# Performance work log

Measured on AMD Instinct MI355X. Metric: run time of the kernel, lower is better.

The kernel has to match this reference:

```python
import jax, jax.numpy as jnp
import numpy as np

TAU_MEM = 20.0
V_THRESH = 1.0
DECAY = float(np.exp(-1.0 / TAU_MEM))
SLOPE = 5.0  # fast-sigmoid surrogate slope


@jax.custom_vjp
def spike(x):
    # Heaviside spike with fast-sigmoid surrogate gradient
    return (x > 0).astype(x.dtype)

def _spike_fwd(x):
    return spike(x), x

def _spike_bwd(x, g):
    surr = 1.0 / (1.0 + SLOPE * jnp.abs(x)) ** 2
    return (g * surr,)

spike.defvjp(_spike_fwd, _spike_bwd)


def setup_inputs() -> dict:
    key = jax.random.key(0)
    k1, k2 = jax.random.split(key)
    B, T, n_in, n_out = 32, 1000, 1024, 512
    input_spikes_seq = (jax.random.uniform(k1, (B, T, n_in)) < 0.05).astype(jnp.float32)
    w_init_scale = 0.5
    W = jax.random.normal(k2, (n_out, n_in), dtype=jnp.float32) * (w_init_scale / np.sqrt(n_in))
    return {"input_spikes_seq": input_spikes_seq, "W": W}


def reference(input_spikes_seq, W):
    # input_spikes_seq: (B, T, n_in); W: (n_out, n_in) -> out: (B, T, n_out)
    B, T, _ = input_spikes_seq.shape
    n_out = W.shape[0]
    # Hoist the GEMM out of the time loop: (B,T,n_in) x (n_out,n_in) -> (B,T,n_out)
    I = jnp.einsum('bti,oi->bto', input_spikes_seq, W)
    I_t = jnp.transpose(I, (1, 0, 2))  # (T, B, n_out)

    def step(v, i_t):
        v = v * DECAY + i_t
        s = spike(v - V_THRESH)
        v = v * (1.0 - jax.lax.stop_gradient(s))  # reset, detached as in torch
        return v, s

    v0 = jnp.zeros((B, n_out), dtype=input_spikes_seq.dtype)
    _, out_t = jax.lax.scan(step, v0, I_t)  # out_t: (T, B, n_out)
    return jnp.transpose(out_t, (1, 0, 2))
```

## Files before the change

kernel.cpp:

```cpp
#include <hip/hip_runtime.h>


#define N_IN   1024
#define N_OUT  512
#define DECAY_F 0.95122942450071400910f
#define SCALE     17179869184.0
#define SCALE_INV 5.8207660913467407e-11f

typedef int  v4i  __attribute__((ext_vector_type(4)));
typedef int  v16i __attribute__((ext_vector_type(16)));

typedef __attribute__((address_space(1))) const void gv_t;
typedef __attribute__((address_space(3))) void lv_t;
__device__ __forceinline__ void gl16(const signed char* g, signed char* l) {
    __builtin_amdgcn_global_load_lds((gv_t*)g, (lv_t*)l, 16, 0, 0);
}

__global__ __launch_bounds__(256) void prep(const float* __restrict__ S,
                                            signed char* __restrict__ S8,
                                            const float* __restrict__ W,
                                            signed char* __restrict__ D8,
                                            int nS16blocks) {
    if ((int)blockIdx.x < nS16blocks) {
        const int g = blockIdx.x * 256 + threadIdx.x;
        const float4* p = reinterpret_cast<const float4*>(S) + (size_t)g * 4;
        union { signed char c[16]; int4 v; } u;
#pragma unroll
        for (int q = 0; q < 4; ++q) {
            const float4 v = p[q];
            u.c[q * 4 + 0] = (signed char)(v.x != 0.f);
            u.c[q * 4 + 1] = (signed char)(v.y != 0.f);
            u.c[q * 4 + 2] = (signed char)(v.z != 0.f);
            u.c[q * 4 + 3] = (signed char)(v.w != 0.f);
        }
        reinterpret_cast<int4*>(S8)[g] = u.v;
    } else {
        const int n  = blockIdx.x - nS16blocks;
        const int k0 = threadIdx.x * 4;
        const float4 wv = *reinterpret_cast<const float4*>(W + (size_t)n * N_IN + k0);
        const float ww[4] = {wv.x, wv.y, wv.z, wv.w};
        int pk[4] = {0, 0, 0, 0};
#pragma unroll
        for (int j = 0; j < 4; ++j) {
            long long wi = (long long)rint((double)ww[j] * SCALE);
            const int d0 = (int)((wi + 128) & 255) - 128; wi = (wi - d0) >> 8;
            const int d1 = (int)((wi + 128) & 255) - 128; wi = (wi - d1) >> 8;
            const int d2 = (int)((wi + 128) & 255) - 128; wi = (wi - d2) >> 8;
            const int d3 = (int)wi;
            pk[0] |= (d0 & 255) << (8 * j);
            pk[1] |= (d1 & 255) << (8 * j);
            pk[2] |= (d2 & 255) << (8 * j);
            pk[3] |= (d3 & 255) << (8 * j);
        }
#pragma unroll
        for (int d = 0; d < 4; ++d)
            *reinterpret_cast<int*>(D8 + (size_t)(d * N_OUT + n) * N_IN + k0) = pk[d];
    }
}

#define BM 256
#define BN 64
#define BK 64
#define TILEB (BM * BK)
#define BUFSZ (2 * TILEB)

#define BARRIER __builtin_amdgcn_s_barrier()
#define LGKM0 do { asm volatile("s_waitcnt lgkmcnt(0)" ::: "memory");             \
                   __builtin_amdgcn_sched_barrier(0); } while (0)
#define VMCNT_(n) asm volatile("s_waitcnt vmcnt(" #n ")" ::: "memory")
#define LDV(off) (*reinterpret_cast<const v4i*>(lds + (off)))
#define MFMA_I8 __builtin_amdgcn_mfma_i32_32x32x32_i8

__global__ __launch_bounds__(512, 2) void gemm_i8(
        const signed char* __restrict__ S8,
        const signed char* __restrict__ D8,
        float* __restrict__ I, int M) {
    extern __shared__ signed char lds[];

    const int tid  = threadIdx.x;
    const int lane = tid & 63;
    const int w    = tid >> 6;
    const int wwm  = w >> 1;
    const int wwn  = w & 1;

    const int nx  = M / BM;
    const int u   = (blockIdx.x & 7) * nx + (blockIdx.x >> 3);
    const int bm  = u >> 3;
    const int bn  = u & 7;
    const int m0 = bm * BM;
    const int n0 = bn * BN;

    const int lrow  = lane >> 2;
    const int sslot = (lane & 3) << 4;
    const int swzs  = ((lrow >> 1) & 3) << 4;
    const int scola = sslot ^ swzs;

    const signed char* aSrc0 = S8 + (size_t)(m0 + w * 16 + lrow) * N_IN + scola;
    const signed char* aSrc1 = aSrc0 + (size_t)128 * N_IN;
    const signed char* bSrc0 = D8 + (size_t)((w >> 2) * N_OUT + n0 + (w & 3) * 16 + lrow) * N_IN + scola;
    const signed char* bSrc1 = bSrc0 + (size_t)2 * N_OUT * N_IN;

    const int aDst0 = (w * 16) * 64;
    const int aDst1 = aDst0 + 128 * 64;
    const int bDst0 = TILEB + (w * 16) * 64;
    const int bDst1 = bDst0 + 128 * 64;

    v16i acc[2][4];
#pragma unroll
    for (int mf = 0; mf < 2; ++mf)
#pragma unroll
        for (int d = 0; d < 4; ++d)
#pragma unroll
            for (int i = 0; i < 16; ++i) acc[mf][d][i] = 0;

    const int fr = lane & 31;
    const int kh = (lane >> 5) * 16;
    const int swzr = ((fr >> 1) & 3) << 4;
    const int kx0 = kh ^ swzr;
    const int kx1 = (32 + kh) ^ swzr;
    const int ra0 = (wwm * 64 + fr) * 64;
    const int ra1 = (wwm * 64 + 32 + fr) * 64;
    const int rb0 = (0 * 64 + wwn * 32 + fr) * 64;
    const int rb1 = (1 * 64 + wwn * 32 + fr) * 64;
    const int rb2 = (2 * 64 + wwn * 32 + fr) * 64;
    const int rb3 = (3 * 64 + wwn * 32 + fr) * 64;

#define TILE_STEP(CUR, STG, KT, DOSTAGE, VML)                                     \
    {                                                                             \
        const int base = (CUR) * BUFSZ;                                           \
        v4i af0, af1, bf0, bf1, bf2, bf3;                                         \
                                                           \
        af0 = LDV(base + ra0 + kx0);                                              \
        af1 = LDV(base + ra1 + kx0);                                              \
        bf0 = LDV(base + TILEB + rb0 + kx0);                                      \
        bf1 = LDV(base + TILEB + rb1 + kx0);                                      \
        bf2 = LDV(base + TILEB + rb2 + kx0);                                      \
        bf3 = LDV(base + TILEB + rb3 + kx0);                                      \
        if (DOSTAGE) {                                                            \
            gl16(aSrc0 + (KT + 2) * BK, lds + (STG) * BUFSZ + aDst0);             \
            gl16(aSrc1 + (KT + 2) * BK, lds + (STG) * BUFSZ + aDst1);             \
        }                                                                         \
        LGKM0;                                                                    \
        __builtin_amdgcn_s_setprio(1);                                            \
        acc[0][0] = MFMA_I8(af0, bf0, acc[0][0], 0, 0, 0);                        \
        acc[1][0] = MFMA_I8(af1, bf0, acc[1][0], 0, 0, 0);                        \
        acc[0][1] = MFMA_I8(af0, bf1, acc[0][1], 0, 0, 0);                        \
        acc[1][1] = MFMA_I8(af1, bf1, acc[1][1], 0, 0, 0);                        \
        acc[0][2] = MFMA_I8(af0, bf2, acc[0][2], 0, 0, 0);                        \
        acc[1][2] = MFMA_I8(af1, bf2, acc[1][2], 0, 0, 0);                        \
        acc[0][3] = MFMA_I8(af0, bf3, acc[0][3], 0, 0, 0);                        \
        acc[1][3] = MFMA_I8(af1, bf3, acc[1][3], 0, 0, 0);                        \
        __builtin_amdgcn_s_setprio(0);                                            \
                                                           \
        af0 = LDV(base + ra0 + kx1);                                              \
        af1 = LDV(base + ra1 + kx1);                                              \
        bf0 = LDV(base + TILEB + rb0 + kx1);                                      \
        bf1 = LDV(base + TILEB + rb1 + kx1);                                      \
        bf2 = LDV(base + TILEB + rb2 + kx1);                                      \
        bf3 = LDV(base + TILEB + rb3 + kx1);                                      \
        if (DOSTAGE) {                                                            \
            gl16(bSrc0 + (KT + 2) * BK, lds + (STG) * BUFSZ + bDst0);             \
            gl16(bSrc1 + (KT + 2) * BK, lds + (STG) * BUFSZ + bDst1);             \
        }                                                                         \
        LGKM0;                                                                    \
        __builtin_amdgcn_s_setprio(1);                                            \
        acc[0][0] = MFMA_I8(af0, bf0, acc[0][0], 0, 0, 0);                        \
        acc[1][0] = MFMA_I8(af1, bf0, acc[1][0], 0, 0, 0);                        \
        acc[0][1] = MFMA_I8(af0, bf1, acc[0][1], 0, 0, 0);                        \
        acc[1][1] = MFMA_I8(af1, bf1, acc[1][1], 0, 0, 0);                        \
        acc[0][2] = MFMA_I8(af0, bf2, acc[0][2], 0, 0, 0);                        \
        acc[1][2] = MFMA_I8(af1, bf2, acc[1][2], 0, 0, 0);                        \
        acc[0][3] = MFMA_I8(af0, bf3, acc[0][3], 0, 0, 0);                        \
        acc[1][3] = MFMA_I8(af1, bf3, acc[1][3], 0, 0, 0);                        \
        __builtin_amdgcn_s_setprio(0);                                            \
        VMCNT_(VML);                                                              \
        BARRIER;                                                                  \
    }

    gl16(aSrc0, lds + aDst0);
    gl16(aSrc1, lds + aDst1);
    gl16(bSrc0, lds + bDst0);
    gl16(bSrc1, lds + bDst1);
    gl16(aSrc0 + BK, lds + BUFSZ + aDst0);
    gl16(aSrc1 + BK, lds + BUFSZ + aDst1);
    gl16(bSrc0 + BK, lds + BUFSZ + bDst0);
    gl16(bSrc1 + BK, lds + BUFSZ + bDst1);
    VMCNT_(4);
    BARRIER;

    TILE_STEP(0, 2, 0,  1, 4)
    TILE_STEP(1, 0, 1,  1, 4)
    TILE_STEP(2, 1, 2,  1, 4)
    TILE_STEP(0, 2, 3,  1, 4)
    TILE_STEP(1, 0, 4,  1, 4)
    TILE_STEP(2, 1, 5,  1, 4)
    TILE_STEP(0, 2, 6,  1, 4)
    TILE_STEP(1, 0, 7,  1, 4)
    TILE_STEP(2, 1, 8,  1, 4)
    TILE_STEP(0, 2, 9,  1, 4)
    TILE_STEP(1, 0, 10, 1, 4)
    TILE_STEP(2, 1, 11, 1, 4)
    TILE_STEP(0, 2, 12, 1, 4)
    TILE_STEP(1, 0, 13, 1, 4)
    TILE_STEP(2, 1, 14, 0, 0)
    TILE_STEP(0, 0, 15, 0, 0)

    const int col = fr;
    const int rb_ = (lane >> 5) * 4;
#pragma unroll
    for (int mf = 0; mf < 2; ++mf) {
#pragma unroll
        for (int reg = 0; reg < 16; ++reg) {
            const int row = (reg & 3) + 8 * (reg >> 2) + rb_;
            const long long v =
                ((long long)acc[mf][3][reg] << 24) + ((long long)acc[mf][2][reg] << 16) +
                ((long long)acc[mf][1][reg] << 8) + (long long)acc[mf][0][reg];
            I[(size_t)(m0 + wwm * 64 + mf * 32 + row) * N_OUT + n0 + wwn * 32 + col] =
                (float)v * SCALE_INV;
        }
    }
}
#undef TILE_STEP

#define UT 50
__global__ __launch_bounds__(64) void lif_scan3(float* __restrict__ IO, int T) {
    const int idx = blockIdx.x * 64 + threadIdx.x;
    const int b = idx >> 9, o = idx & (N_OUT - 1);
    float* p = IO + (size_t)b * T * N_OUT + o;
    float ca[UT], cb[UT];
    float v = 0.f;
#pragma unroll
    for (int j = 0; j < UT; ++j) ca[j] = p[(size_t)j * N_OUT];
#pragma unroll 1
    for (int t0 = 0; t0 < T; t0 += 2 * UT) {
        if (t0 + UT < T) {
#pragma unroll
            for (int j = 0; j < UT; ++j) cb[j] = p[(size_t)(t0 + UT + j) * N_OUT];
        }
#pragma unroll
        for (int j = 0; j < UT; ++j) {
            v = v * DECAY_F + ca[j];
            float s = (v > 1.0f) ? 1.0f : 0.f;
            v *= (1.f - s);
            ca[j] = s;
        }
#pragma unroll
        for (int j = 0; j < UT; ++j) p[(size_t)(t0 + j) * N_OUT] = ca[j];
        if (t0 + UT >= T) break;
        if (t0 + 2 * UT < T) {
#pragma unroll
            for (int j = 0; j < UT; ++j) ca[j] = p[(size_t)(t0 + 2 * UT + j) * N_OUT];
        }
#pragma unroll
        for (int j = 0; j < UT; ++j) {
            v = v * DECAY_F + cb[j];
            float s = (v > 1.0f) ? 1.0f : 0.f;
            v *= (1.f - s);
            cb[j] = s;
        }
#pragma unroll
        for (int j = 0; j < UT; ++j) p[(size_t)(t0 + UT + j) * N_OUT] = cb[j];
    }
}

__global__ __launch_bounds__(256) void transpose_w(const float* __restrict__ W,
                                                   float* __restrict__ WT) {
    __shared__ float t[32][33];
    const int k0 = blockIdx.x * 32;
    const int n0 = blockIdx.y * 32;
    const int lx = threadIdx.x & 31;
    const int ly = threadIdx.x >> 5;
#pragma unroll
    for (int r = ly; r < 32; r += 8)
        t[r][lx] = W[(size_t)(n0 + r) * N_IN + k0 + lx];
    __syncthreads();
#pragma unroll
    for (int r = ly; r < 32; r += 8)
        WT[(size_t)(k0 + r) * N_OUT + n0 + lx] = t[lx][r];
}

__global__ __launch_bounds__(256) void gather_rows(
        const float* __restrict__ S, const float* __restrict__ WT,
        float* __restrict__ I, int M) {
    const int wid  = blockIdx.x * 4 + (threadIdx.x >> 6);
    const int lane = threadIdx.x & 63;
    if (wid >= M) return;
    const float* srow = S + (size_t)wid * N_IN;
    float4 a0 = {0.f, 0.f, 0.f, 0.f};
    float4 a1 = {0.f, 0.f, 0.f, 0.f};
    float sv[16];
#pragma unroll
    for (int g = 0; g < 16; ++g) sv[g] = srow[g * 64 + lane];
#pragma unroll
    for (int g = 0; g < 16; ++g) {
        unsigned long long m = __ballot(sv[g] != 0.0f);
        while (m) {
            const int bb = __builtin_ctzll(m);
            m &= m - 1;
            const int k = g * 64 + bb;
            const float* wp = WT + (size_t)k * N_OUT + lane * 4;
            const float4 w0 = *reinterpret_cast<const float4*>(wp);
            const float4 w1 = *reinterpret_cast<const float4*>(wp + 256);
            a0.x += w0.x; a0.y += w0.y; a0.z += w0.z; a0.w += w0.w;
            a1.x += w1.x; a1.y += w1.y; a1.z += w1.z; a1.w += w1.w;
        }
    }
    float* op = I + (size_t)wid * N_OUT + lane * 4;
    *reinterpret_cast<float4*>(op) = a0;
    *reinterpret_cast<float4*>(op + 256) = a1;
}

extern "C" void kernel_launch(void* const* d_in, const int* in_sizes, int n_in,
                              void* d_out, int out_size, void* d_ws, size_t ws_size,
                              hipStream_t stream) {
    const float* S = (const float*)d_in[0];
    const float* W = (const float*)d_in[1];
    float* out = (float*)d_out;

    const int K = N_IN;
    const int M = in_sizes[0] / K;
    const int B = 32;
    const int T = M / B;

    const size_t s8_bytes = (size_t)M * N_IN;
    const size_t d8_bytes = (size_t)4 * N_OUT * N_IN;
    const size_t need = s8_bytes + d8_bytes;

    if (ws_size >= need && (M % BM) == 0 && ((M / BM) * (N_OUT / BN)) % 8 == 0) {
        signed char* S8 = (signed char*)d_ws;
        signed char* D8 = (signed char*)d_ws + s8_bytes;
        const int nS16blocks = (M * N_IN / 16) / 256;
        prep<<<nS16blocks + N_OUT, 256, 0, stream>>>(S, S8, W, D8, nS16blocks);
        const size_t lds_bytes = (size_t)3 * BUFSZ;
        gemm_i8<<<(M / BM) * (N_OUT / BN), 512, lds_bytes, stream>>>(S8, D8, out, M);
        lif_scan3<<<(B * N_OUT) / 64, 64, 0, stream>>>(out, T);
    } else if (ws_size >= (size_t)N_IN * N_OUT * sizeof(float) && (M % 4) == 0) {
        float* WT = (float*)d_ws;
        dim3 tg(N_IN / 32, N_OUT / 32);
        transpose_w<<<tg, 256, 0, stream>>>(W, WT);
        gather_rows<<<M / 4, 256, 0, stream>>>(S, WT, out, M);
        lif_scan3<<<(B * N_OUT) / 64, 64, 0, stream>>>(out, T);
    }
}
```

Baseline: 140.5 us.

## Split weights into three int8 digits instead of four to cut MFMA work

Lowers the fixed-point weight scale from 2^34 to 2^26, so each weight splits into three signed int8 digits instead of four. The B tile shrinks to 192 rows, the MFMA count per K-step drops by a quarter, and one global load per wave in the upper half of the block is skipped. The LDS fragment loads are also reordered: both K-halves are issued up front and a partial lgkmcnt wait lets the first MFMA batch start earlier. Weight quantisation becomes coarser (resolution about 1.5e-8), which could flip spikes whose membrane potential sits right at threshold.

```diff
diff --git a/kernel.cpp b/kernel.cpp
--- a/kernel.cpp
+++ b/kernel.cpp
@@ -4,8 +4,8 @@
 #define N_IN   1024
 #define N_OUT  512
 #define DECAY_F 0.95122942450071400910f
-#define SCALE     17179869184.0
-#define SCALE_INV 5.8207660913467407e-11f
+#define SCALE     67108864.0
+#define SCALE_INV 1.4901161193847656e-08f
 
 typedef int  v4i  __attribute__((ext_vector_type(4)));
 typedef int  v16i __attribute__((ext_vector_type(16)));
@@ -39,21 +39,19 @@
         const int k0 = threadIdx.x * 4;
         const float4 wv = *reinterpret_cast<const float4*>(W + (size_t)n * N_IN + k0);
         const float ww[4] = {wv.x, wv.y, wv.z, wv.w};
-        int pk[4] = {0, 0, 0, 0};
+        int pk[3] = {0, 0, 0};
 #pragma unroll
         for (int j = 0; j < 4; ++j) {
             long long wi = (long long)rint((double)ww[j] * SCALE);
             const int d0 = (int)((wi + 128) & 255) - 128; wi = (wi - d0) >> 8;
             const int d1 = (int)((wi + 128) & 255) - 128; wi = (wi - d1) >> 8;
-            const int d2 = (int)((wi + 128) & 255) - 128; wi = (wi - d2) >> 8;
-            const int d3 = (int)wi;
+            const int d2 = (int)wi;
             pk[0] |= (d0 & 255) << (8 * j);
             pk[1] |= (d1 & 255) << (8 * j);
             pk[2] |= (d2 & 255) << (8 * j);
-            pk[3] |= (d3 & 255) << (8 * j);
-        }
-#pragma unroll
-        for (int d = 0; d < 4; ++d)
+        }
+#pragma unroll
+        for (int d = 0; d < 3; ++d)
             *reinterpret_cast<int*>(D8 + (size_t)(d * N_OUT + n) * N_IN + k0) = pk[d];
     }
 }
@@ -61,13 +59,15 @@
 #define BM 256
 #define BN 64
 #define BK 64
-#define TILEB (BM * BK)
-#define BUFSZ (2 * TILEB)
+#define ATILE (BM * BK)
+#define BTILE (192 * BK)
+#define BUFSZ (ATILE + BTILE)
 
 #define BARRIER __builtin_amdgcn_s_barrier()
-#define LGKM0 do { asm volatile("s_waitcnt lgkmcnt(0)" ::: "memory");             \
-                   __builtin_amdgcn_sched_barrier(0); } while (0)
+#define SB0 __builtin_amdgcn_sched_barrier(0)
+#define LGKM(n) do { asm volatile("s_waitcnt lgkmcnt(" #n ")" ::: "memory"); SB0; } while (0)
 #define VMCNT_(n) asm volatile("s_waitcnt vmcnt(" #n ")" ::: "memory")
+#define VMC do { if (w < 4) VMCNT_(4); else VMCNT_(3); } while (0)
 #define LDV(off) (*reinterpret_cast<const v4i*>(lds + (off)))
 #define MFMA_I8 __builtin_amdgcn_mfma_i32_32x32x32_i8
 
@@ -102,14 +102,14 @@
 
     const int aDst0 = (w * 16) * 64;
     const int aDst1 = aDst0 + 128 * 64;
-    const int bDst0 = TILEB + (w * 16) * 64;
+    const int bDst0 = ATILE + (w * 16) * 64;
     const int bDst1 = bDst0 + 128 * 64;
 
-    v16i acc[2][4];
+    v16i acc[2][3];
 #pragma unroll
     for (int mf = 0; mf < 2; ++mf)
 #pragma unroll
-        for (int d = 0; d < 4; ++d)
+        for (int d = 0; d < 3; ++d)
 #pragma unroll
             for (int i = 0; i < 16; ++i) acc[mf][d][i] = 0;
 
@@ -123,87 +123,81 @@
     const int rb0 = (0 * 64 + wwn * 32 + fr) * 64;
     const int rb1 = (1 * 64 + wwn * 32 + fr) * 64;
     const int rb2 = (2 * 64 + wwn * 32 + fr) * 64;
-    const int rb3 = (3 * 64 + wwn * 32 + fr) * 64;
-
-#define TILE_STEP(CUR, STG, KT, DOSTAGE, VML)                                     \
+
+#define TILE_STEP(CUR, STG, KT, DOSTAGE)                                          \
     {                                                                             \
         const int base = (CUR) * BUFSZ;                                           \
-        v4i af0, af1, bf0, bf1, bf2, bf3;                                         \
-                                                           \
-        af0 = LDV(base + ra0 + kx0);                                              \
-        af1 = LDV(base + ra1 + kx0);                                              \
-        bf0 = LDV(base + TILEB + rb0 + kx0);                                      \
-        bf1 = LDV(base + TILEB + rb1 + kx0);                                      \
-        bf2 = LDV(base + TILEB + rb2 + kx0);                                      \
-        bf3 = LDV(base + TILEB + rb3 + kx0);                                      \
+        v4i xa0, xa1, xb0, xb1, xb2;                                              \
+        v4i ya0, ya1, yb0, yb1, yb2;                                              \
+        xa0 = LDV(base + ra0 + kx0);                                              \
+        xa1 = LDV(base + ra1 + kx0);                                              \
+        xb0 = LDV(base + ATILE + rb0 + kx0);                                      \
+        xb1 = LDV(base + ATILE + rb1 + kx0);                                      \
+        xb2 = LDV(base + ATILE + rb2 + kx0);                                      \
+        SB0;                                                                      \
+        ya0 = LDV(base + ra0 + kx1);                                              \
+        ya1 = LDV(base + ra1 + kx1);                                              \
+        yb0 = LDV(base + ATILE + rb0 + kx1);                                      \
+        yb1 = LDV(base + ATILE + rb1 + kx1);                                      \
+        yb2 = LDV(base + ATILE + rb2 + kx1);                                      \
+        SB0;                                                                      \
+        LGKM(5);                                                                  \
         if (DOSTAGE) {                                                            \
             gl16(aSrc0 + (KT + 2) * BK, lds + (STG) * BUFSZ + aDst0);             \
             gl16(aSrc1 + (KT + 2) * BK, lds + (STG) * BUFSZ + aDst1);             \
         }                                                                         \
-        LGKM0;                                                                    \
         __builtin_amdgcn_s_setprio(1);                                            \
-        acc[0][0] = MFMA_I8(af0, bf0, acc[0][0], 0, 0, 0);                        \
-        acc[1][0] = MFMA_I8(af1, bf0, acc[1][0], 0, 0, 0);                        \
-        acc[0][1] = MFMA_I8(af0, bf1, acc[0][1], 0, 0, 0);                        \
-        acc[1][1] = MFMA_I8(af1, bf1, acc[1][1], 0, 0, 0);                        \
-        acc[0][2] = MFMA_I8(af0, bf2, acc[0][2], 0, 0, 0);                        \
-        acc[1][2] = MFMA_I8(af1, bf2, acc[1][2], 0, 0, 0);                        \
-        acc[0][3] = MFMA_I8(af0, bf3, acc[0][3], 0, 0, 0);                        \
-        acc[1][3] = MFMA_I8(af1, bf3, acc[1][3], 0, 0, 0);                        \
+        acc[0][0] = MFMA_I8(xa0, xb0, acc[0][0], 0, 0, 0);                        \
+        acc[1][0] = MFMA_I8(xa1, xb0, acc[1][0], 0, 0, 0);                        \
+        acc[0][1] = MFMA_I8(xa0, xb1, acc[0][1], 0, 0, 0);                        \
+        acc[1][1] = MFMA_I8(xa1, xb1, acc[1][1], 0, 0, 0);                        \
+        acc[0][2] = MFMA_I8(xa0, xb2, acc[0][2], 0, 0, 0);                        \
+        acc[1][2] = MFMA_I8(xa1, xb2, acc[1][2], 0, 0, 0);                        \
         __builtin_amdgcn_s_setprio(0);                                            \
-                                                           \
-        af0 = LDV(base + ra0 + kx1);                                              \
-        af1 = LDV(base + ra1 + kx1);                                              \
-        bf0 = LDV(base + TILEB + rb0 + kx1);                                      \
-        bf1 = LDV(base + TILEB + rb1 + kx1);                                      \
-        bf2 = LDV(base + TILEB + rb2 + kx1);                                      \
-        bf3 = LDV(base + TILEB + rb3 + kx1);                                      \
         if (DOSTAGE) {                                                            \
             gl16(bSrc0 + (KT + 2) * BK, lds + (STG) * BUFSZ + bDst0);             \
-            gl16(bSrc1 + (KT + 2) * BK, lds + (STG) * BUFSZ + bDst1);             \
+            if (w < 4) gl16(bSrc1 + (KT + 2) * BK, lds + (STG) * BUFSZ + bDst1);  \
         }                                                                         \
-        LGKM0;                                                                    \
+        LGKM(0);                                                                  \
         __builtin_amdgcn_s_setprio(1);                                            \
-        acc[0][0] = MFMA_I8(af0, bf0, acc[0][0], 0, 0, 0);                        \
-        acc[1][0] = MFMA_I8(af1, bf0, acc[1][0], 0, 0, 0);                        \
-        acc[0][1] = MFMA_I8(af0, bf1, acc[0][1], 0, 0, 0);                        \
-        acc[1][1] = MFMA_I8(af1, bf1, acc[1][1], 0, 0, 0);                        \
-        acc[0][2] = MFMA_I8(af0, bf2, acc[0][2], 0, 0, 0);                        \
-        acc[1][2] = MFMA_I8(af1, bf2, acc[1][2], 0, 0, 0);                        \
-        acc[0][3] = MFMA_I8(af0, bf3, acc[0][3], 0, 0, 0);                        \
-        acc[1][3] = MFMA_I8(af1, bf3, acc[1][3], 0, 0, 0);                        \
+        acc[0][0] = MFMA_I8(ya0, yb0, acc[0][0], 0, 0, 0);                        \
+        acc[1][0] = MFMA_I8(ya1, yb0, acc[1][0], 0, 0, 0);                        \
+        acc[0][1] = MFMA_I8(ya0, yb1, acc[0][1], 0, 0, 0);                        \
+        acc[1][1] = MFMA_I8(ya1, yb1, acc[1][1], 0, 0, 0);                        \
+        acc[0][2] = MFMA_I8(ya0, yb2, acc[0][2], 0, 0, 0);                        \
+        acc[1][2] = MFMA_I8(ya1, yb2, acc[1][2], 0, 0, 0);                        \
         __builtin_amdgcn_s_setprio(0);                                            \
-        VMCNT_(VML);                                                              \
+        if (DOSTAGE) { VMC; } else { VMCNT_(0); }                                 \
         BARRIER;                                                                  \
     }
 
     gl16(aSrc0, lds + aDst0);
     gl16(aSrc1, lds + aDst1);
     gl16(bSrc0, lds + bDst0);
-    gl16(bSrc1, lds + bDst1);
+    if (w < 4) gl16(bSrc1, lds + bDst1);
     gl16(aSrc0 + BK, lds + BUFSZ + aDst0);
     gl16(aSrc1 + BK, lds + BUFSZ + aDst1);
     gl16(bSrc0 + BK, lds + BUFSZ + bDst0);
-    gl16(bSrc1 + BK, lds + BUFSZ + bDst1);
-    VMCNT_(4);
+    if (w < 4) gl16(bSrc1 + BK, lds + BUFSZ + bDst1);
+    VMC;
     BARRIER;
 
-    TILE_STEP(0, 2, 0,  1, 4)
-    TILE_STEP(1, 0, 1,  1, 4)
-    TILE_STEP(2, 1, 2,  1, 4)
-    TILE_STEP(0, 2, 3,  1, 4)
-    TILE_STEP(1, 0, 4,  1, 4)
-    TILE_STEP(2, 1, 5,  1, 4)
-    TILE_STEP(0, 2, 6,  1, 4)
-    TILE_STEP(1, 0, 7,  1, 4)
-    TILE_STEP(2, 1, 8,  1, 4)
-    TILE_STEP(0, 2, 9,  1, 4)
-    TILE_STEP(1, 0, 10, 1, 4)
-    TILE_STEP(2, 1, 11, 1, 4)
-    TILE_STEP(0, 2, 12, 1, 4)
-    TILE_STEP(1, 0, 13, 1, 4)
-    TILE_STEP(2, 1, 14, 0, 0)
-    TILE_STEP(0, 0, 15, 0, 0)
+    TILE_STEP(0, 2, 0,  1)
+    TILE_STEP(1, 0, 1,  1)
+    TILE_STEP(2, 1, 2,  1)
+    TILE_STEP(0, 2, 3,  1)
+    TILE_STEP(1, 0, 4,  1)
+    TILE_STEP(2, 1, 5,  1)
+    TILE_STEP(0, 2, 6,  1)
+    TILE_STEP(1, 0, 7,  1)
+    TILE_STEP(2, 1, 8,  1)
+    TILE_STEP(0, 2, 9,  1)
+    TILE_STEP(1, 0, 10, 1)
+    TILE_STEP(2, 1, 11, 1)
+    TILE_STEP(0, 2, 12, 1)
+    TILE_STEP(1, 0, 13, 1)
+    TILE_STEP(2, 1, 14, 0)
+    TILE_STEP(0, 0, 15, 0)
 
     const int col = fr;
     const int rb_ = (lane >> 5) * 4;
@@ -213,7 +207,7 @@
         for (int reg = 0; reg < 16; ++reg) {
             const int row = (reg & 3) + 8 * (reg >> 2) + rb_;
             const long long v =
-                ((long long)acc[mf][3][reg] << 24) + ((long long)acc[mf][2][reg] << 16) +
+                ((long long)acc[mf][2][reg] << 16) +
                 ((long long)acc[mf][1][reg] << 8) + (long long)acc[mf][0][reg];
             I[(size_t)(m0 + wwm * 64 + mf * 32 + row) * N_OUT + n0 + wwn * 32 + col] =
                 (float)v * SCALE_INV;
@@ -323,7 +317,7 @@
     const int T = M / B;
 
     const size_t s8_bytes = (size_t)M * N_IN;
-    const size_t d8_bytes = (size_t)4 * N_OUT * N_IN;
+    const size_t d8_bytes = (size_t)3 * N_OUT * N_IN;
     const size_t need = s8_bytes + d8_bytes;
 
     if (ws_size >= need && (M % BM) == 0 && ((M / BM) * (N_OUT / BN)) % 8 == 0) {
```

Result: faster. 126.7 us (median of 2 runs) (-9.8%).
